# Kernel tuning notes

Measured on AMD Instinct MI355X. Metric: run time of the kernel, lower is better.

The kernel has to match this reference:

```python
import jax, jax.numpy as jnp
import numpy as np

CODEBOOK_SIZE = 8192
EMBED_DIM = 128
BETA = 0.25


def setup_inputs() -> dict:
    key = jax.random.key(0)
    k1, k2 = jax.random.split(key)
    z = jax.random.normal(k1, (8, 4096, EMBED_DIM), dtype=jnp.float32)
    # nn.Embedding weight init: uniform(-1/embedding_dim, 1/embedding_dim)
    emb = jax.random.uniform(
        k2, (CODEBOOK_SIZE, EMBED_DIM), dtype=jnp.float32,
        minval=-1.0 / EMBED_DIM, maxval=1.0 / EMBED_DIM)
    return {"z": z, "emb": emb}


def reference(z, emb):
    sg = jax.lax.stop_gradient
    zf = z.reshape(-1, EMBED_DIM)                      # [N, D]
    # squared-distance: |z|^2 + |e|^2 - 2 z.e^T  -> [N, K]
    d = (jnp.sum(zf * zf, axis=1, keepdims=True)
         + jnp.sum(emb * emb, axis=1)
         - 2.0 * jnp.einsum('nd,kd->nk', zf, emb))
    idx = jnp.argmin(d, axis=1)                        # [N]
    z_q = emb[idx].reshape(z.shape)                    # gather + reshape

    # codebook usage perplexity (bincount)
    counts = jnp.zeros(CODEBOOK_SIZE, dtype=jnp.float32).at[idx].add(1.0)
    e_mean = counts / idx.size
    perplexity = jnp.exp(-jnp.sum(e_mean * jnp.log(e_mean + 1e-8)))

    commit_loss = (BETA * jnp.mean((sg(z_q) - z) ** 2)
                   + jnp.mean((z_q - sg(z)) ** 2))
    z_q_st = z + sg(z_q - z)                           # straight-through
    return z_q_st, commit_loss, perplexity
```

## Files before the change

kernel.cpp:

```cpp
#include <hip/hip_runtime.h>
#include <float.h>
#include <math.h>

#define DIM    128
#define KCB    8192
#define BT     128
#define NC     128
#define NCHUNK (KCB / NC)
#define CAP    32
#define MARGIN 0.016f

typedef __attribute__((ext_vector_type(8))) short bf16x8;
typedef __attribute__((ext_vector_type(4))) float f32x4;

__device__ unsigned g_eh[KCB * DIM / 2];
__device__ float    g_h[KCB];
__device__ unsigned g_counts[KCB];
__device__ double   g_loss;
__device__ unsigned g_done;

__device__ __forceinline__ unsigned short f2b(float x) {
    union { float f; unsigned u; } v; v.f = x;
    unsigned r = v.u + 0x7fffu + ((v.u >> 16) & 1u);
    return (unsigned short)(r >> 16);
}
__device__ __forceinline__ void gll16(const void* g, void* l) {
    __builtin_amdgcn_global_load_lds(
        (const __attribute__((address_space(1))) void*)g,
        (__attribute__((address_space(3))) void*)l, 16, 0, 0);
}
__device__ __forceinline__ unsigned pkey(float sc, int c) {
    unsigned u = __float_as_uint(sc);
    u ^= (unsigned)(((int)u >> 31)) | 0x80000000u;
    return (u & ~8191u) | (unsigned)c;
}
__device__ __forceinline__ float key2sc(unsigned k) {
    unsigned u = (k & 0x80000000u) ? (k ^ 0x80000000u) : ~k;
    return __uint_as_float(u);
}

__global__ __launch_bounds__(256) void vq_prep(const float* __restrict__ emb)
{
    const int tid = threadIdx.x;
    const int gid = blockIdx.x * 256 + tid;
    if (gid < KCB) g_counts[gid] = 0u;
    if (gid == 0)  { g_loss = 0.0; g_done = 0u; }

    const int code = (blockIdx.x << 2) + (tid >> 6);
    const int lane = tid & 63;
    const float2 v = ((const float2*)emb)[code * 64 + lane];

    unsigned short h0 = f2b(v.x), h1 = f2b(v.y);
    const int chunk = code >> 7, r = code & 127;
    const int n   = r >> 4,  l15r = r & 15;
    const int kk  = lane >> 4, lg = (lane >> 2) & 3, wib = lane & 3;
    const int widx = chunk * 8192 + n * 1024 + kk * 256 + lg * 64 + l15r * 4 + wib;
    g_eh[widx] = (unsigned)h0 | ((unsigned)h1 << 16);

    float s = v.x * v.x + v.y * v.y;
    #pragma unroll
    for (int o = 32; o > 0; o >>= 1) s += __shfl_down(s, o);
    if (lane == 0) g_h[code] = 0.5f * s;
}

__global__ __launch_bounds__(1024) void vq_main(
    const float* __restrict__ z, const float* __restrict__ emb, float* __restrict__ out)
{
    __shared__ char     smem[2 * 32768];
    __shared__ unsigned rv[BT * 4];
    __shared__ unsigned bk_sh[BT];
    __shared__ int      lcnt[BT];
    __shared__ int      list[BT * CAP];
    __shared__ int      idx_sh[BT];
    __shared__ double   wred[16];
    __shared__ int      done_sh;

    const int tid  = threadIdx.x;
    const int lane = tid & 63;
    const int wid  = tid >> 6;
    const int tq   = wid >> 2;
    const int cq   = wid & 3;
    const int l15  = lane & 15;
    const int lg   = lane >> 4;
    const long t0  = (long)blockIdx.x * BT;

    bf16x8 ah[2][4];
    #pragma unroll
    for (int m = 0; m < 2; ++m) {
        const long trow = t0 + tq * 32 + m * 16 + l15;
        #pragma unroll
        for (int kk = 0; kk < 4; ++kk) {
            const float4* zp = (const float4*)(z + trow * DIM + kk * 32 + lg * 8);
            float4 v0 = zp[0], v1 = zp[1];
            float xs[8] = {v0.x, v0.y, v0.z, v0.w, v1.x, v1.y, v1.z, v1.w};
            #pragma unroll
            for (int j = 0; j < 8; ++j) ah[m][kk][j] = (short)f2b(xs[j]);
        }
    }

    const int rbase = cq * 8192 + (lane << 4);

    unsigned b0[2][4], b1[2][4];
    #pragma unroll
    for (int m = 0; m < 2; ++m)
        #pragma unroll
        for (int r = 0; r < 4; ++r) { b0[m][r] = 0xFFFFFFFFu; b1[m][r] = 0xFFFFFFFFu; }

    {
        const int o = tid * 16;
        gll16((const char*)g_eh + o, smem + o);
        gll16((const char*)g_eh + 16384 + o, smem + 16384 + o);
    }
    __syncthreads();

    for (int ch = 0; ch < NCHUNK; ++ch) {
        const int cur = ch & 1;
        if (ch + 1 < NCHUNK) {
            const int  o  = tid * 16;
            const long go = (long)(ch + 1) * 32768;
            char* ldst = smem + (cur ^ 1) * 32768;
            gll16((const char*)g_eh + go + o, ldst + o);
            gll16((const char*)g_eh + go + 16384 + o, ldst + 16384 + o);
        }

        const char* base = smem + cur * 32768 + rbase;
        const int   c0   = ch * NC + cq * 32 + l15;
        const float hv0  = g_h[c0];
        const float hv1  = g_h[c0 + 16];

        #pragma unroll
        for (int n = 0; n < 2; ++n) {
            bf16x8 bh[4];
            #pragma unroll
            for (int kk = 0; kk < 4; ++kk)
                bh[kk] = *(const bf16x8*)(base + n * 4096 + kk * 1024);
            f32x4 acc[2];
            #pragma unroll
            for (int m = 0; m < 2; ++m) acc[m] = (f32x4){0.f, 0.f, 0.f, 0.f};
            #pragma unroll
            for (int kk = 0; kk < 4; ++kk)
                #pragma unroll
                for (int m = 0; m < 2; ++m)
                    acc[m] = __builtin_amdgcn_mfma_f32_16x16x32_bf16(ah[m][kk], bh[kk], acc[m], 0, 0, 0);

            const float hvn = n ? hv1 : hv0;
            const int   c   = c0 + n * 16;
            #pragma unroll
            for (int m = 0; m < 2; ++m)
                #pragma unroll
                for (int r = 0; r < 4; ++r) {
                    unsigned k  = pkey(hvn - acc[m][r], c);
                    unsigned mx = max(b0[m][r], k);
                    b0[m][r] = min(b0[m][r], k);
                    b1[m][r] = min(b1[m][r], mx);
                }
        }
        __syncthreads();
    }

    #pragma unroll
    for (int m = 0; m < 2; ++m)
        #pragma unroll
        for (int r = 0; r < 4; ++r) {
            unsigned k = b0[m][r];
            #pragma unroll
            for (int o = 1; o < 16; o <<= 1) k = min(k, (unsigned)__shfl_xor((int)k, o));
            if (l15 == 0) rv[(tq * 32 + m * 16 + lg * 4 + r) * 4 + cq] = k;
        }
    __syncthreads();
    if (tid < BT) {
        unsigned k = min(min(rv[tid * 4], rv[tid * 4 + 1]), min(rv[tid * 4 + 2], rv[tid * 4 + 3]));
        bk_sh[tid] = k;
        lcnt[tid]  = 0;
    }
    __syncthreads();

    #pragma unroll
    for (int m = 0; m < 2; ++m)
        #pragma unroll
        for (int r = 0; r < 4; ++r) {
            const int   t  = tq * 32 + m * 16 + lg * 4 + r;
            const float th = key2sc(bk_sh[t]) + MARGIN;
            if (key2sc(b0[m][r]) <= th) {
                int p = atomicAdd(&lcnt[t], 1);
                if (p < CAP) list[t * CAP + p] = (int)(b0[m][r] & 8191u);
            }
            if (key2sc(b1[m][r]) <= th) {
                int p = atomicAdd(&lcnt[t], 1);
                if (p < CAP) list[t * CAP + p] = (int)(b1[m][r] & 8191u);
            }
        }
    __syncthreads();

    {
        const int t  = wid * 8 + (lane >> 3);
        const int li = lane & 7;
        const int cnt = min(lcnt[t], CAP);
        const float4* zt = (const float4*)(z + (t0 + t) * DIM) + li * 4;
        float4 zr0 = zt[0], zr1 = zt[1], zr2 = zt[2], zr3 = zt[3];
        float bsc = FLT_MAX; int bidx = KCB;
        for (int j = 0; j < cnt; ++j) {
            const int c = list[t * CAP + j];
            const float4* ec = (const float4*)(emb + (size_t)c * DIM) + li * 4;
            float4 e0 = ec[0], e1 = ec[1], e2 = ec[2], e3 = ec[3];
            float s = zr0.x*e0.x + zr0.y*e0.y + zr0.z*e0.z + zr0.w*e0.w
                    + zr1.x*e1.x + zr1.y*e1.y + zr1.z*e1.z + zr1.w*e1.w
                    + zr2.x*e2.x + zr2.y*e2.y + zr2.z*e2.z + zr2.w*e2.w
                    + zr3.x*e3.x + zr3.y*e3.y + zr3.z*e3.z + zr3.w*e3.w;
            #pragma unroll
            for (int o = 1; o < 8; o <<= 1) s += __shfl_xor(s, o);
            float sc = g_h[c] - s;
            if (sc < bsc || (sc == bsc && c < bidx)) { bsc = sc; bidx = c; }
        }
        if (li == 0) {
            idx_sh[t] = bidx;
            atomicAdd(&g_counts[bidx], 1u);
        }
    }
    __syncthreads();

    float lsum = 0.f;
    {
        const float4* zf4 = (const float4*)(z + t0 * DIM);
        const float4* ef4 = (const float4*)emb;
        float4*       of4 = (float4*)(out + t0 * DIM);
        #pragma unroll
        for (int r = 0; r < 4; ++r) {
            int f = r * 1024 + tid;
            int t = f >> 5, dw = f & 31;
            int ci = idx_sh[t];
            float4 e4 = ef4[(size_t)ci * 32 + dw];
            float4 z4 = zf4[f];
            float dx = e4.x - z4.x, dy = e4.y - z4.y;
            float dz = e4.z - z4.z, dw2 = e4.w - z4.w;
            lsum += dx * dx + dy * dy + dz * dz + dw2 * dw2;
            float4 o;
            o.x = z4.x + dx; o.y = z4.y + dy; o.z = z4.z + dz; o.w = z4.w + dw2;
            of4[f] = o;
        }
    }
    #pragma unroll
    for (int o = 32; o > 0; o >>= 1) lsum += __shfl_down(lsum, o);
    if (lane == 0) wred[wid] = (double)lsum;
    __syncthreads();
    if (tid == 0) {
        double s = 0.0;
        #pragma unroll
        for (int w = 0; w < 16; ++w) s += wred[w];
        atomicAdd(&g_loss, s);
    }

    __threadfence();
    if (tid == 0) done_sh = (atomicAdd(&g_done, 1u) == gridDim.x - 1) ? 1 : 0;
    __syncthreads();
    if (done_sh) {
        const int ntok    = (int)gridDim.x * BT;
        const int n_elems = ntok * DIM;
        double s = 0.0;
        for (int i = tid; i < KCB; i += 1024) {
            unsigned cnt = atomicAdd(&g_counts[i], 0u);
            float em = (float)cnt / (float)ntok;
            s += (double)(em * logf(em + 1e-8f));
        }
        #pragma unroll
        for (int o = 32; o > 0; o >>= 1) s += __shfl_down(s, o);
        if (lane == 0) wred[wid] = s;
        __syncthreads();
        if (tid == 0) {
            double tot = 0.0;
            #pragma unroll
            for (int w = 0; w < 16; ++w) tot += wred[w];
            double L = atomicAdd(&g_loss, 0.0);
            out[(size_t)n_elems]     = (float)(1.25 * L / (double)n_elems);
            out[(size_t)n_elems + 1] = expf((float)(-tot));
        }
    }
}

extern "C" void kernel_launch(void* const* d_in, const int* in_sizes, int n_in,
                              void* d_out, int out_size, void* d_ws, size_t ws_size,
                              hipStream_t stream)
{
    const float* z   = (const float*)d_in[0];
    const float* emb = (const float*)d_in[1];
    float* out = (float*)d_out;

    const int n_elems = in_sizes[0];
    const int ntok    = n_elems / DIM;

    vq_prep<<<dim3(KCB / 4),   256,  0, stream>>>(emb);
    vq_main<<<dim3(ntok / BT), 1024, 0, stream>>>(z, emb, out);
}
```

Before: 314.5 us.

## Load codebook fragments directly from global into registers, dropping LDS staging

Replaces the double-buffered global-to-LDS staging of the bf16 codebook with per-wave direct global loads into registers, prefetching the next chunk into a second register set. This removes the per-chunk block barrier and the LDS reads. In exchange, four waves per block now redundantly fetch the same codebook fragments from L2, and register pressure rises under the 1024-thread launch bound.

Result: faster. 292.9 us (-6.9%).

```diff
diff --git a/kernel.cpp b/kernel.cpp
--- a/kernel.cpp
+++ b/kernel.cpp
@@ -24,11 +24,6 @@
     unsigned r = v.u + 0x7fffu + ((v.u >> 16) & 1u);
     return (unsigned short)(r >> 16);
 }
-__device__ __forceinline__ void gll16(const void* g, void* l) {
-    __builtin_amdgcn_global_load_lds(
-        (const __attribute__((address_space(1))) void*)g,
-        (__attribute__((address_space(3))) void*)l, 16, 0, 0);
-}
 __device__ __forceinline__ unsigned pkey(float sc, int c) {
     unsigned u = __float_as_uint(sc);
     u ^= (unsigned)(((int)u >> 31)) | 0x80000000u;
@@ -66,7 +61,6 @@
 __global__ __launch_bounds__(1024) void vq_main(
     const float* __restrict__ z, const float* __restrict__ emb, float* __restrict__ out)
 {
-    __shared__ char     smem[2 * 32768];
     __shared__ unsigned rv[BT * 4];
     __shared__ unsigned bk_sh[BT];
     __shared__ int      lcnt[BT];
@@ -98,42 +92,31 @@
         }
     }
 
-    const int rbase = cq * 8192 + (lane << 4);
-
     unsigned b0[2][4], b1[2][4];
     #pragma unroll
     for (int m = 0; m < 2; ++m)
         #pragma unroll
         for (int r = 0; r < 4; ++r) { b0[m][r] = 0xFFFFFFFFu; b1[m][r] = 0xFFFFFFFFu; }
 
-    {
-        const int o = tid * 16;
-        gll16((const char*)g_eh + o, smem + o);
-        gll16((const char*)g_eh + 16384 + o, smem + 16384 + o);
-    }
-    __syncthreads();
+    const char* gbase = (const char*)g_eh + cq * 8192 + (lane << 4);
+
+    bf16x8 bcur[8], bnxt[8];
+    #pragma unroll
+    for (int j = 0; j < 8; ++j) bcur[j] = *(const bf16x8*)(gbase + j * 1024);
 
     for (int ch = 0; ch < NCHUNK; ++ch) {
-        const int cur = ch & 1;
         if (ch + 1 < NCHUNK) {
-            const int  o  = tid * 16;
-            const long go = (long)(ch + 1) * 32768;
-            char* ldst = smem + (cur ^ 1) * 32768;
-            gll16((const char*)g_eh + go + o, ldst + o);
-            gll16((const char*)g_eh + go + 16384 + o, ldst + 16384 + o);
-        }
-
-        const char* base = smem + cur * 32768 + rbase;
-        const int   c0   = ch * NC + cq * 32 + l15;
-        const float hv0  = g_h[c0];
-        const float hv1  = g_h[c0 + 16];
+            const char* gn = gbase + (long)(ch + 1) * 32768;
+            #pragma unroll
+            for (int j = 0; j < 8; ++j) bnxt[j] = *(const bf16x8*)(gn + j * 1024);
+        }
+
+        const int   c0  = ch * NC + cq * 32 + l15;
+        const float hv0 = g_h[c0];
+        const float hv1 = g_h[c0 + 16];
 
         #pragma unroll
         for (int n = 0; n < 2; ++n) {
-            bf16x8 bh[4];
-            #pragma unroll
-            for (int kk = 0; kk < 4; ++kk)
-                bh[kk] = *(const bf16x8*)(base + n * 4096 + kk * 1024);
             f32x4 acc[2];
             #pragma unroll
             for (int m = 0; m < 2; ++m) acc[m] = (f32x4){0.f, 0.f, 0.f, 0.f};
@@ -141,7 +124,7 @@
             for (int kk = 0; kk < 4; ++kk)
                 #pragma unroll
                 for (int m = 0; m < 2; ++m)
-                    acc[m] = __builtin_amdgcn_mfma_f32_16x16x32_bf16(ah[m][kk], bh[kk], acc[m], 0, 0, 0);
+                    acc[m] = __builtin_amdgcn_mfma_f32_16x16x32_bf16(ah[m][kk], bcur[n * 4 + kk], acc[m], 0, 0, 0);
 
             const float hvn = n ? hv1 : hv0;
             const int   c   = c0 + n * 16;
@@ -155,7 +138,8 @@
                     b1[m][r] = min(b1[m][r], mx);
                 }
         }
-        __syncthreads();
+        #pragma unroll
+        for (int j = 0; j < 8; ++j) bcur[j] = bnxt[j];
     }
 
     #pragma unroll
```
